# Performance work log

Hardware: AMD Instinct MI355X
Metric: run time of the kernel (lower is better)

The kernel has to match this reference:

```python
import jax, jax.numpy as jnp
import numpy as np

GX, GY, GZ = 128, 128, 16   # voxel_range
N = 100000                  # occupied voxels
C = 64                      # channels (inc == outc)
K = 27                      # 3x3x3 kernel offsets
EPS = 1e-5
NEG_SLOPE = 0.01            # LeakyReLU default


def _kernel_map():
    """Build sparse-conv neighbor map: nbr[k, n] = row index of the input voxel at
    coord[n] + offset[k], or N (sentinel -> zero feature) if unoccupied/out of range."""
    rng = np.random.RandomState(0)
    flat = rng.choice(GX * GY * GZ, size=N, replace=False)
    x = flat // (GY * GZ)
    rem = flat % (GY * GZ)
    y = rem // GZ
    z = rem % GZ
    lut = np.full(GX * GY * GZ, N, dtype=np.int32)
    lut[flat] = np.arange(N, dtype=np.int32)
    offs = [(i, j, k) for i in (-1, 0, 1) for j in (-1, 0, 1) for k in (-1, 0, 1)]
    nbr = np.full((K, N), N, dtype=np.int32)
    for ki, (dx, dy, dz) in enumerate(offs):
        xs, ys, zs = x + dx, y + dy, z + dz
        valid = (xs >= 0) & (xs < GX) & (ys >= 0) & (ys < GY) & (zs >= 0) & (zs < GZ)
        fl = (np.clip(xs, 0, GX - 1) * (GY * GZ)
              + np.clip(ys, 0, GY - 1) * GZ
              + np.clip(zs, 0, GZ - 1))
        nbr[ki] = np.where(valid, lut[fl], N)
    return jnp.asarray(nbr)


def setup_inputs() -> dict:
    key = jax.random.key(0)
    k0, k1, k2 = jax.random.split(key, 3)
    w_scale = 1.0 / np.sqrt(C * K)  # Minkowski-style fan-in init
    return {
        "feats": jax.random.normal(k0, (N, C), jnp.float32),
        "W1": jax.random.normal(k1, (K, C, C), jnp.float32) * w_scale,
        "g1": jnp.ones((C,), jnp.float32),
        "b1": jnp.zeros((C,), jnp.float32),
        "W2": jax.random.normal(k2, (K, C, C), jnp.float32) * w_scale,
        "g2": jnp.ones((C,), jnp.float32),
        "b2": jnp.zeros((C,), jnp.float32),
        "nbr_idx": _kernel_map(),
    }


def _sparse_conv(f, W, nbr):
    # gather-GEMM-scatter: fp has a zero sentinel row at index N
    fp = jnp.concatenate([f, jnp.zeros((1, f.shape[1]), f.dtype)], axis=0)
    g = fp[nbr]                                # [K, N, Cin] gathered neighbors
    return jnp.einsum('knc,kco->no', g, W)     # [N, Cout]


def _bn(x, gamma, beta):
    # training-mode BatchNorm over all active voxels, per channel
    m = jnp.mean(x, axis=0)
    v = jnp.var(x, axis=0)
    return (x - m) * jax.lax.rsqrt(v + EPS) * gamma + beta


def _lrelu(x):
    return jnp.where(x >= 0, x, NEG_SLOPE * x)


def reference(feats, W1, g1, b1, W2, g2, b2, nbr_idx):
    skip = feats  # downsample is identity (inc == outc, stride == 1)
    y = _lrelu(_bn(_sparse_conv(feats, W1, nbr_idx), g1, b1))
    y = _lrelu(_bn(_sparse_conv(y, W2, nbr_idx), g2, b2))
    return _lrelu(skip + y)
```

## Files before the change

### kernel.cpp

```cpp
#include <hip/hip_runtime.h>
#include <hip/hip_bf16.h>


#define N_VOX 100000
#define NCH 64
#define NK 27
#define ROWS 128
#define NBLK ((N_VOX + ROWS - 1) / ROWS)

typedef __hip_bfloat16 bf16;
typedef __attribute__((ext_vector_type(8))) short bf16x8;
typedef __attribute__((ext_vector_type(4))) float f32x4;

__device__ __forceinline__ float b2f(short s) {
  unsigned u = ((unsigned)(unsigned short)s) << 16;
  return __builtin_bit_cast(float, u);
}
__device__ __forceinline__ short f2b(float f) {
  __hip_bfloat16 h = __float2bfloat16(f);
  return __builtin_bit_cast(short, h);
}

__device__ __forceinline__ void gload16(const void* g, void* l) {
  __builtin_amdgcn_global_load_lds(
      (const __attribute__((address_space(1))) void*)g,
      (__attribute__((address_space(3))) void*)l, 16, 0, 0);
}

__global__ void cast_feats(const float* __restrict__ feats, bf16* __restrict__ fbf) {
  const size_t i = ((size_t)blockIdx.x * 256 + threadIdx.x) * 8;
  if (i >= (size_t)(N_VOX + 1) * NCH) return;
  bf16x8 o;
  if (i < (size_t)N_VOX * NCH) {
    const f32x4 v0 = *reinterpret_cast<const f32x4*>(feats + i);
    const f32x4 v1 = *reinterpret_cast<const f32x4*>(feats + i + 4);
#pragma unroll
    for (int e = 0; e < 8; ++e) o[e] = f2b(e < 4 ? v0[e] : v1[e - 4]);
  } else {
#pragma unroll
    for (int e = 0; e < 8; ++e) o[e] = 0;
  }
  *reinterpret_cast<bf16x8*>((short*)fbf + i) = o;
}

__global__ void pack_w(const float* __restrict__ W1, const float* __restrict__ W2,
                       bf16* __restrict__ wp1, bf16* __restrict__ wp2) {
  const int t = blockIdx.x * 256 + threadIdx.x;
  const int half = NK * 4 * 2 * 64;
  if (t >= 2 * half) return;
  const float* W = (t < half) ? W1 : W2;
  short* wp = (short*)((t < half) ? wp1 : wp2);
  const int q = (t < half) ? t : t - half;
  const int l  = q & 63;
  const int kb = (q >> 6) & 1;
  const int j  = (q >> 7) & 3;
  const int k  = q >> 9;
  const int oo = j * 16 + (l & 15);
  const int c0 = kb * 32 + (l >> 4) * 8;
  bf16x8 v;
#pragma unroll
  for (int e = 0; e < 8; ++e)
    v[e] = f2b(W[((size_t)k * 64 + c0 + e) * 64 + oo]);
  *reinterpret_cast<bf16x8*>(&wp[(size_t)q * 8]) = v;
}

__global__ __launch_bounds__(256, 4)
void conv_mfma(const bf16* __restrict__ feat, const bf16* __restrict__ wp,
               const int* __restrict__ nbr, bf16* __restrict__ y,
               float* __restrict__ part) {
  __shared__ short GB[3][8 * 512];
  __shared__ int nbrL[NK * ROWS];
  __shared__ float redS[4][NCH];
  __shared__ float redQ[4][NCH];

  const int tid = threadIdx.x;
  const int lane = tid & 63;
  const int wv = tid >> 6;

  const int nwg = NBLK;
  const int xcd = blockIdx.x & 7;
  const int pos = blockIdx.x >> 3;
  const int q8 = nwg >> 3, r8 = nwg & 7;
  const int bid = (xcd < r8 ? xcd * (q8 + 1) : r8 * (q8 + 1) + (xcd - r8) * q8) + pos;
  const int n0 = bid * ROWS;

  for (int t = tid; t < NK * ROWS; t += 256) {
    const int k = t >> 7;
    const int rr = t & (ROWS - 1);
    nbrL[t] = (n0 + rr < N_VOX) ? nbr[(size_t)k * N_VOX + n0 + rr] : N_VOX;
  }
  __syncthreads();

  const int r0 = wv * 32 + (lane & 15);
  const int koff = (lane >> 4) * 8;

  f32x4 acc[2][4];
#pragma unroll
  for (int h = 0; h < 2; ++h)
#pragma unroll
    for (int j = 0; j < 4; ++j)
      acc[h][j] = (f32x4){0.f, 0.f, 0.f, 0.f};

  bf16x8 AE[4], AO[4];

#define LOAD_A(A, k)                                                        \
  {                                                                         \
    const int i0 = nbrL[(k) * ROWS + r0];                                   \
    const int i1 = nbrL[(k) * ROWS + r0 + 16];                              \
    A[0] = *reinterpret_cast<const bf16x8*>(feat + (size_t)i0 * 64 + koff); \
    A[1] = *reinterpret_cast<const bf16x8*>(feat + (size_t)i0 * 64 + 32 + koff); \
    A[2] = *reinterpret_cast<const bf16x8*>(feat + (size_t)i1 * 64 + koff); \
    A[3] = *reinterpret_cast<const bf16x8*>(feat + (size_t)i1 * 64 + 32 + koff); \
  }

#define STAGE_B(slot, k)                                                    \
  {                                                                         \
    const short* srcb = (const short*)wp + (size_t)(k) * 4096 +             \
                        (wv * 2) * 512 + lane * 8;                          \
    gload16((const void*)srcb, (void*)&GB[slot][(wv * 2) * 512]);           \
    gload16((const void*)(srcb + 512), (void*)&GB[slot][(wv * 2 + 1) * 512]); \
  }

#define MFMA_TAP(A, B)                                                      \
  _Pragma("unroll")                                                         \
  for (int h = 0; h < 2; ++h)                                               \
    _Pragma("unroll")                                                       \
    for (int j = 0; j < 4; ++j)                                             \
      _Pragma("unroll")                                                     \
      for (int kb = 0; kb < 2; ++kb)                                        \
        acc[h][j] = __builtin_amdgcn_mfma_f32_16x16x32_bf16(                \
            A[h * 2 + kb], B[j * 2 + kb], acc[h][j], 0, 0, 0);

#define TILE_STEP(Acur, Aoth, t, cur)                                       \
  {                                                                         \
    asm volatile("s_waitcnt vmcnt(2)" ::: "memory");                        \
    __builtin_amdgcn_sched_barrier(0);                                      \
    __builtin_amdgcn_s_barrier();                                           \
    LOAD_A(Aoth, (t) + 1)                                                   \
    if ((t) <= NK - 3) {                                                    \
      const int stslot = (cur) >= 1 ? (cur) - 1 : 2;           \
      STAGE_B(stslot, (t) + 2)                                              \
    }                                                                       \
    __builtin_amdgcn_sched_barrier(0);       \
    bf16x8 Bf[8];                                                           \
    _Pragma("unroll")                                                       \
    for (int f = 0; f < 8; ++f)                                             \
      Bf[f] = *reinterpret_cast<const bf16x8*>(&GB[cur][f * 512 + lane * 8]); \
    MFMA_TAP(Acur, Bf)                                                      \
  }

  STAGE_B(0, 0)
  LOAD_A(AE, 0)
  STAGE_B(1, 1)

  int cur = 0;
#pragma unroll 1
  for (int j = 0; j < 13; ++j) {
    const int t = 2 * j;
    TILE_STEP(AE, AO, t, cur)
    cur = (cur == 2) ? 0 : cur + 1;
    TILE_STEP(AO, AE, t + 1, cur)
    cur = (cur == 2) ? 0 : cur + 1;
  }
  {
    asm volatile("s_waitcnt vmcnt(0)" ::: "memory");
    __builtin_amdgcn_sched_barrier(0);
    __builtin_amdgcn_s_barrier();
    bf16x8 Bf[8];
#pragma unroll
    for (int f = 0; f < 8; ++f)
      Bf[f] = *reinterpret_cast<const bf16x8*>(&GB[2][f * 512 + lane * 8]);
    MFMA_TAP(AE, Bf)
  }

#undef LOAD_A
#undef STAGE_B
#undef MFMA_TAP
#undef TILE_STEP

#pragma unroll
  for (int h = 0; h < 2; ++h)
#pragma unroll
    for (int j = 0; j < 4; ++j) {
      const int col = j * 16 + (lane & 15);
#pragma unroll
      for (int r = 0; r < 4; ++r) {
        const int row = n0 + wv * 32 + h * 16 + (lane >> 4) * 4 + r;
        if (row < N_VOX) ((short*)y)[(size_t)row * NCH + col] = f2b(acc[h][j][r]);
      }
    }

#pragma unroll
  for (int j = 0; j < 4; ++j) {
    float s1 = 0.f, s2 = 0.f;
#pragma unroll
    for (int h = 0; h < 2; ++h)
#pragma unroll
      for (int r = 0; r < 4; ++r) {
        const float v = acc[h][j][r];
        s1 += v;
        s2 += v * v;
      }
    s1 += __shfl_xor(s1, 16); s2 += __shfl_xor(s2, 16);
    s1 += __shfl_xor(s1, 32); s2 += __shfl_xor(s2, 32);
    if (lane < 16) {
      redS[wv][j * 16 + lane] = s1;
      redQ[wv][j * 16 + lane] = s2;
    }
  }
  __syncthreads();
  if (tid < NCH) {
    const float s1 = redS[0][tid] + redS[1][tid] + redS[2][tid] + redS[3][tid];
    const float s2 = redQ[0][tid] + redQ[1][tid] + redQ[2][tid] + redQ[3][tid];
    part[(size_t)blockIdx.x * 128 + tid] = s1;
    part[(size_t)blockIdx.x * 128 + 64 + tid] = s2;
  }
}

__global__ void finalize(const float* __restrict__ part, int nblk,
                         const float* __restrict__ g, const float* __restrict__ b,
                         float* __restrict__ ab) {
  __shared__ float r1[256], r2[256];
  const int c = blockIdx.x;
  const int t = threadIdx.x;
  float s1 = 0.f, s2 = 0.f;
  for (int bb = t; bb < nblk; bb += 256) {
    s1 += part[(size_t)bb * 128 + c];
    s2 += part[(size_t)bb * 128 + 64 + c];
  }
  r1[t] = s1; r2[t] = s2;
  __syncthreads();
  for (int off = 128; off > 0; off >>= 1) {
    if (t < off) { r1[t] += r1[t + off]; r2[t] += r2[t + off]; }
    __syncthreads();
  }
  if (t == 0) {
    const float m = r1[0] / (float)N_VOX;
    const float v = r2[0] / (float)N_VOX - m * m;
    const float a = g[c] * rsqrtf(v + 1e-5f);
    const float sh = b[c] - m * a;
    ab[c] = a;
    ab[64 + c] = sh;
  }
}

__global__ void bn_act(const bf16* __restrict__ y, const float* __restrict__ ab,
                       bf16* __restrict__ z) {
  const size_t i = ((size_t)blockIdx.x * 256 + threadIdx.x) * 8;
  if (i >= (size_t)(N_VOX + 1) * NCH) return;
  const int col = (int)(i & 63);
  bf16x8 o;
  if (i < (size_t)N_VOX * NCH) {
    const bf16x8 v = *reinterpret_cast<const bf16x8*>((const short*)y + i);
#pragma unroll
    for (int e = 0; e < 8; ++e) {
      float x = b2f(v[e]) * ab[col + e] + ab[64 + col + e];
      x = x < 0.f ? 0.01f * x : x;
      o[e] = f2b(x);
    }
  } else {
#pragma unroll
    for (int e = 0; e < 8; ++e) o[e] = 0;
  }
  *reinterpret_cast<bf16x8*>((short*)z + i) = o;
}

__global__ void bn_act_res(const bf16* __restrict__ y, const float* __restrict__ ab,
                           const float* __restrict__ feats, float* __restrict__ out) {
  const size_t i = ((size_t)blockIdx.x * 256 + threadIdx.x) * 8;
  const int col = (int)(i & 63);
  const bf16x8 v = *reinterpret_cast<const bf16x8*>((const short*)y + i);
  const f32x4 s0 = *reinterpret_cast<const f32x4*>(feats + i);
  const f32x4 s1 = *reinterpret_cast<const f32x4*>(feats + i + 4);
  f32x4 o0, o1;
#pragma unroll
  for (int e = 0; e < 8; ++e) {
    float x = b2f(v[e]) * ab[col + e] + ab[64 + col + e];
    x = x < 0.f ? 0.01f * x : x;
    float r = (e < 4 ? s0[e] : s1[e - 4]) + x;
    r = r < 0.f ? 0.01f * r : r;
    if (e < 4) o0[e] = r; else o1[e - 4] = r;
  }
  *reinterpret_cast<f32x4*>(out + i) = o0;
  *reinterpret_cast<f32x4*>(out + i + 4) = o1;
}

extern "C" void kernel_launch(void* const* d_in, const int* in_sizes, int n_in,
                              void* d_out, int out_size, void* d_ws, size_t ws_size,
                              hipStream_t stream) {
  const float* feats = (const float*)d_in[0];
  const float* W1 = (const float*)d_in[1];
  const float* g1 = (const float*)d_in[2];
  const float* b1 = (const float*)d_in[3];
  const float* W2 = (const float*)d_in[4];
  const float* g2 = (const float*)d_in[5];
  const float* b2 = (const float*)d_in[6];
  const int* nbr = (const int*)d_in[7];
  float* out = (float*)d_out;

  char* p = (char*)d_ws;
  bf16* fbf = (bf16*)p; p += (size_t)(N_VOX + 1) * NCH * 2;
  bf16* ybf = (bf16*)p; p += (size_t)N_VOX * NCH * 2;
  bf16* z = (bf16*)p;   p += (size_t)(N_VOX + 1) * NCH * 2;
  bf16* wp1 = (bf16*)p; p += 442368;
  bf16* wp2 = (bf16*)p; p += 442368;
  float* part = (float*)p; p += (size_t)NBLK * 128 * 4;
  float* ab1 = (float*)p; p += 512;
  float* ab2 = (float*)p; p += 512;

  const int cast_blocks = (int)(((size_t)(N_VOX + 1) * NCH / 8 + 255) / 256);

  cast_feats<<<cast_blocks, 256, 0, stream>>>(feats, fbf);
  pack_w<<<108, 256, 0, stream>>>(W1, W2, wp1, wp2);

  conv_mfma<<<NBLK, 256, 0, stream>>>(fbf, wp1, nbr, ybf, part);
  finalize<<<64, 256, 0, stream>>>(part, NBLK, g1, b1, ab1);
  bn_act<<<cast_blocks, 256, 0, stream>>>(ybf, ab1, z);

  conv_mfma<<<NBLK, 256, 0, stream>>>(z, wp2, nbr, ybf, part);
  finalize<<<64, 256, 0, stream>>>(part, NBLK, g2, b2, ab2);
  bn_act_res<<<(N_VOX * NCH / 8) / 256, 256, 0, stream>>>(ybf, ab2, feats, out);
}
```

Before: 134.7 us.

## Preload all neighbor byte offsets into registers and fully unroll tap pipeline

```diff
diff --git a/kernel.cpp b/kernel.cpp
--- a/kernel.cpp
+++ b/kernel.cpp
@@ -64,14 +64,15 @@
   *reinterpret_cast<bf16x8*>(&wp[(size_t)q * 8]) = v;
 }
 
-__global__ __launch_bounds__(256, 4)
+struct RedT { float S[4][NCH]; float Q[4][NCH]; };
+union SmemU { int offL[NK * ROWS]; RedT red; };
+
+__global__ __launch_bounds__(256, 3)
 void conv_mfma(const bf16* __restrict__ feat, const bf16* __restrict__ wp,
                const int* __restrict__ nbr, bf16* __restrict__ y,
                float* __restrict__ part) {
-  __shared__ short GB[3][8 * 512];
-  __shared__ int nbrL[NK * ROWS];
-  __shared__ float redS[4][NCH];
-  __shared__ float redQ[4][NCH];
+  __shared__ short GB[3][4096];
+  __shared__ SmemU U;
 
   const int tid = threadIdx.x;
   const int lane = tid & 63;
@@ -87,12 +88,23 @@
   for (int t = tid; t < NK * ROWS; t += 256) {
     const int k = t >> 7;
     const int rr = t & (ROWS - 1);
-    nbrL[t] = (n0 + rr < N_VOX) ? nbr[(size_t)k * N_VOX + n0 + rr] : N_VOX;
+    const int idx = (n0 + rr < N_VOX) ? nbr[(size_t)k * N_VOX + n0 + rr] : N_VOX;
+    U.offL[t] = idx << 7;
   }
   __syncthreads();
 
   const int r0 = wv * 32 + (lane & 15);
-  const int koff = (lane >> 4) * 8;
+  const unsigned ko16 = (unsigned)((lane >> 4) * 16);
+
+#define DECL27(M) M(0) M(1) M(2) M(3) M(4) M(5) M(6) M(7) M(8) M(9) M(10) \
+  M(11) M(12) M(13) M(14) M(15) M(16) M(17) M(18) M(19) M(20) M(21) M(22) \
+  M(23) M(24) M(25) M(26)
+#define DECL_VO(t) unsigned vo##t##a, vo##t##b;
+  DECL27(DECL_VO)
+#define PRE_VO(t) \
+  vo##t##a = (unsigned)U.offL[(t) * ROWS + r0] + ko16; \
+  vo##t##b = (unsigned)U.offL[(t) * ROWS + r0 + 16] + ko16;
+  DECL27(PRE_VO)
 
   f32x4 acc[2][4];
 #pragma unroll
@@ -102,15 +114,14 @@
       acc[h][j] = (f32x4){0.f, 0.f, 0.f, 0.f};
 
   bf16x8 AE[4], AO[4];
-
-#define LOAD_A(A, k)                                                        \
+  const char* fbase = (const char*)feat;
+
+#define LOAD_A_(A, va, vb)                                                  \
   {                                                                         \
-    const int i0 = nbrL[(k) * ROWS + r0];                                   \
-    const int i1 = nbrL[(k) * ROWS + r0 + 16];                              \
-    A[0] = *reinterpret_cast<const bf16x8*>(feat + (size_t)i0 * 64 + koff); \
-    A[1] = *reinterpret_cast<const bf16x8*>(feat + (size_t)i0 * 64 + 32 + koff); \
-    A[2] = *reinterpret_cast<const bf16x8*>(feat + (size_t)i1 * 64 + koff); \
-    A[3] = *reinterpret_cast<const bf16x8*>(feat + (size_t)i1 * 64 + 32 + koff); \
+    A[0] = *reinterpret_cast<const bf16x8*>(fbase + (size_t)(va));          \
+    A[1] = *reinterpret_cast<const bf16x8*>(fbase + (size_t)(va) + 64);     \
+    A[2] = *reinterpret_cast<const bf16x8*>(fbase + (size_t)(vb));          \
+    A[3] = *reinterpret_cast<const bf16x8*>(fbase + (size_t)(vb) + 64);     \
   }
 
 #define STAGE_B(slot, k)                                                    \
@@ -131,52 +142,79 @@
         acc[h][j] = __builtin_amdgcn_mfma_f32_16x16x32_bf16(                \
             A[h * 2 + kb], B[j * 2 + kb], acc[h][j], 0, 0, 0);
 
-#define TILE_STEP(Acur, Aoth, t, cur)                                       \
+#define READ_B(Bf, slot)                                                    \
+  bf16x8 Bf[8];                                                             \
+  _Pragma("unroll")                                                         \
+  for (int f = 0; f < 8; ++f)                                               \
+    Bf[f] = *reinterpret_cast<const bf16x8*>(&GB[slot][f * 512 + lane * 8]);
+
+#define TILE(Acur, Aoth, vna, vnb, rdslot, stslot, kstg)                    \
   {                                                                         \
     asm volatile("s_waitcnt vmcnt(2)" ::: "memory");                        \
     __builtin_amdgcn_sched_barrier(0);                                      \
     __builtin_amdgcn_s_barrier();                                           \
-    LOAD_A(Aoth, (t) + 1)                                                   \
-    if ((t) <= NK - 3) {                                                    \
-      const int stslot = (cur) >= 1 ? (cur) - 1 : 2;           \
-      STAGE_B(stslot, (t) + 2)                                              \
-    }                                                                       \
-    __builtin_amdgcn_sched_barrier(0);       \
-    bf16x8 Bf[8];                                                           \
-    _Pragma("unroll")                                                       \
-    for (int f = 0; f < 8; ++f)                                             \
-      Bf[f] = *reinterpret_cast<const bf16x8*>(&GB[cur][f * 512 + lane * 8]); \
+    LOAD_A_(Aoth, vna, vnb)                                                 \
+    STAGE_B(stslot, kstg)                                                   \
+    __builtin_amdgcn_sched_barrier(0);                                      \
+    READ_B(Bf, rdslot)                                                      \
     MFMA_TAP(Acur, Bf)                                                      \
   }
 
   STAGE_B(0, 0)
-  LOAD_A(AE, 0)
+  LOAD_A_(AE, vo0a, vo0b)
   STAGE_B(1, 1)
 
-  int cur = 0;
-#pragma unroll 1
-  for (int j = 0; j < 13; ++j) {
-    const int t = 2 * j;
-    TILE_STEP(AE, AO, t, cur)
-    cur = (cur == 2) ? 0 : cur + 1;
-    TILE_STEP(AO, AE, t + 1, cur)
-    cur = (cur == 2) ? 0 : cur + 1;
+  TILE(AE, AO, vo1a, vo1b, 0, 2, 2)
+  TILE(AO, AE, vo2a, vo2b, 1, 0, 3)
+  TILE(AE, AO, vo3a, vo3b, 2, 1, 4)
+  TILE(AO, AE, vo4a, vo4b, 0, 2, 5)
+  TILE(AE, AO, vo5a, vo5b, 1, 0, 6)
+  TILE(AO, AE, vo6a, vo6b, 2, 1, 7)
+  TILE(AE, AO, vo7a, vo7b, 0, 2, 8)
+  TILE(AO, AE, vo8a, vo8b, 1, 0, 9)
+  TILE(AE, AO, vo9a, vo9b, 2, 1, 10)
+  TILE(AO, AE, vo10a, vo10b, 0, 2, 11)
+  TILE(AE, AO, vo11a, vo11b, 1, 0, 12)
+  TILE(AO, AE, vo12a, vo12b, 2, 1, 13)
+  TILE(AE, AO, vo13a, vo13b, 0, 2, 14)
+  TILE(AO, AE, vo14a, vo14b, 1, 0, 15)
+  TILE(AE, AO, vo15a, vo15b, 2, 1, 16)
+  TILE(AO, AE, vo16a, vo16b, 0, 2, 17)
+  TILE(AE, AO, vo17a, vo17b, 1, 0, 18)
+  TILE(AO, AE, vo18a, vo18b, 2, 1, 19)
+  TILE(AE, AO, vo19a, vo19b, 0, 2, 20)
+  TILE(AO, AE, vo20a, vo20b, 1, 0, 21)
+  TILE(AE, AO, vo21a, vo21b, 2, 1, 22)
+  TILE(AO, AE, vo22a, vo22b, 0, 2, 23)
+  TILE(AE, AO, vo23a, vo23b, 1, 0, 24)
+  TILE(AO, AE, vo24a, vo24b, 2, 1, 25)
+  TILE(AE, AO, vo25a, vo25b, 0, 2, 26)
+  {
+    asm volatile("s_waitcnt vmcnt(2)" ::: "memory");
+    __builtin_amdgcn_sched_barrier(0);
+    __builtin_amdgcn_s_barrier();
+    LOAD_A_(AE, vo26a, vo26b)
+    __builtin_amdgcn_sched_barrier(0);
+    READ_B(Bf, 1)
+    MFMA_TAP(AO, Bf)
   }
   {
     asm volatile("s_waitcnt vmcnt(0)" ::: "memory");
     __builtin_amdgcn_sched_barrier(0);
     __builtin_amdgcn_s_barrier();
-    bf16x8 Bf[8];
-#pragma unroll
-    for (int f = 0; f < 8; ++f)
-      Bf[f] = *reinterpret_cast<const bf16x8*>(&GB[2][f * 512 + lane * 8]);
+    __builtin_amdgcn_sched_barrier(0);
+    READ_B(Bf, 2)
     MFMA_TAP(AE, Bf)
   }
 
-#undef LOAD_A
+#undef DECL27
+#undef DECL_VO
+#undef PRE_VO
+#undef LOAD_A_
 #undef STAGE_B
 #undef MFMA_TAP
-#undef TILE_STEP
+#undef READ_B
+#undef TILE
 
 #pragma unroll
   for (int h = 0; h < 2; ++h)
@@ -190,6 +228,7 @@
       }
     }
 
+  __syncthreads();
 #pragma unroll
   for (int j = 0; j < 4; ++j) {
     float s1 = 0.f, s2 = 0.f;
@@ -204,14 +243,14 @@
     s1 += __shfl_xor(s1, 16); s2 += __shfl_xor(s2, 16);
     s1 += __shfl_xor(s1, 32); s2 += __shfl_xor(s2, 32);
     if (lane < 16) {
-      redS[wv][j * 16 + lane] = s1;
-      redQ[wv][j * 16 + lane] = s2;
+      U.red.S[wv][j * 16 + lane] = s1;
+      U.red.Q[wv][j * 16 + lane] = s2;
     }
   }
   __syncthreads();
   if (tid < NCH) {
-    const float s1 = redS[0][tid] + redS[1][tid] + redS[2][tid] + redS[3][tid];
-    const float s2 = redQ[0][tid] + redQ[1][tid] + redQ[2][tid] + redQ[3][tid];
+    const float s1 = U.red.S[0][tid] + U.red.S[1][tid] + U.red.S[2][tid] + U.red.S[3][tid];
+    const float s2 = U.red.Q[0][tid] + U.red.Q[1][tid] + U.red.Q[2][tid] + U.red.Q[3][tid];
     part[(size_t)blockIdx.x * 128 + tid] = s1;
     part[(size_t)blockIdx.x * 128 + 64 + tid] = s2;
   }
```

Measured after the change: 160.4 us. 19.0% more time.
